# Performance work log

Measured on AMD Instinct MI355X. Metric: run time of the kernel, lower is better.

## Reference

```python
import jax, jax.numpy as jnp
import numpy as np

EPS = 1e-3  # keras LayerNormalization default epsilon


def layer_norm(x, gamma, beta):
    mu = jnp.mean(x, axis=-1, keepdims=True)
    var = jnp.mean(jnp.square(x - mu), axis=-1, keepdims=True)
    return gamma * (x - mu) * jax.lax.rsqrt(var + EPS) + beta


def setup_inputs() -> dict:
    key = jax.random.key(0)
    ks = jax.random.split(key, 5)
    B, T, E, H = 2, 2048, 64, 8
    glorot = lambda k, shape, fan_in, fan_out: jax.random.normal(k, shape, jnp.float32) * np.sqrt(2.0 / (fan_in + fan_out))
    return {
        "embedding": jax.random.normal(ks[0], (B, T, E), jnp.float32),
        "key_kernel": glorot(ks[1], (1, H, E), H, E),
        "query_kernel": glorot(ks[2], (1, H, E), H, E),
        "value_kernel": glorot(ks[3], (1, H, E, E), E, E),
        "ff_kernel": glorot(ks[4], (1, H, H, E, E), H * E, H * E),
        "ln1_gamma": jnp.ones((E,), jnp.float32),
        "ln1_beta": jnp.zeros((E,), jnp.float32),
        "ln2_gamma": jnp.ones((E,), jnp.float32),
        "ln2_beta": jnp.zeros((E,), jnp.float32),
    }


def reference(embedding, key_kernel, query_kernel, value_kernel, ff_kernel,
              ln1_gamma, ln1_beta, ln2_gamma, ln2_beta):
    # embedding: [B,T,E]; token input is expanded to [B,1,T,E] and broadcast over heads.
    kk, qk = key_kernel[0], query_kernel[0]          # [H,E]
    vk, fk = value_kernel[0], ff_kernel[0]           # [H,E,E], [H,H,E,E]
    k = jnp.einsum('bte,he->bht', embedding, kk)     # rank-1 key score per token
    q = jnp.einsum('bte,he->bht', embedding, qk)
    v = jnp.einsum('bte,hef->bhtf', embedding, vk)   # [B,H,T,E]
    scores = jnp.einsum('bhq,bhk->bhqk', q, k)       # rank-1 outer-product scores [B,H,T,T]
    attn = jax.nn.softmax(scores, axis=-1)
    z = jnp.einsum('bhqk,bhke->bhqe', attn, v)       # [B,H,T,E]
    z = embedding[:, None, :, :] + z                 # residual (broadcast over heads)
    z = layer_norm(z, ln1_gamma, ln1_beta)
    y = jnp.einsum('bhte,hgef->bgtf', z, fk)         # cross-head FFN, contracts H and E
    y = z + y
    y = jax.nn.gelu(y, approximate=True)             # tfa GELU default approximate=True
    return layer_norm(y, ln2_gamma, ln2_beta)        # [B,H,T,E]
```

## Files before the change

kernel.cpp:

```cpp
#include <hip/hip_runtime.h>
#include <math.h>

#define T 2048
#define E 64
#define H 8
#define B 2

typedef __attribute__((ext_vector_type(4))) float f32x4;
typedef __attribute__((ext_vector_type(8))) short s16x8;

static __device__ __forceinline__ unsigned short f2bf(float x) {
    union { float f; unsigned u; } v; v.f = x;
    unsigned r = v.u + 0x7FFFu + ((v.u >> 16) & 1u);
    return (unsigned short)(r >> 16);
}
static __device__ __forceinline__ float bf2f(unsigned short u) {
    union { unsigned u; float f; } v; v.u = ((unsigned)u) << 16;
    return v.f;
}
static __device__ __forceinline__ unsigned pk_bf16(float lo, float hi) {
    unsigned r;
    asm("v_cvt_pk_bf16_f32 %0, %1, %2" : "=v"(r) : "v"(lo), "v"(hi));
    return r;
}

__global__ __launch_bounds__(256) void qkvT_kernel(
    const float* __restrict__ emb,
    const float* __restrict__ qk,
    const float* __restrict__ kk,
    const float* __restrict__ vk,
    float* __restrict__ qs,
    float* __restrict__ ks,
    unsigned short* __restrict__ vT)
{
    int h  = blockIdx.x & 7;
    int tc = blockIdx.x >> 3;
    int b  = tc >> 5;
    int t0 = (tc & 31) * 64;
    int tid = threadIdx.x;

    __shared__ __align__(16) float eL[64][64];
    __shared__ __align__(16) float wkT[64*68];
    __shared__ __align__(16) unsigned short vtile[4096];

    #pragma unroll
    for (int i = 0; i < 4; ++i) {
        int s = tid + i*256;
        int t = s >> 4, e4 = s & 15;
        ((float4*)&eL[t][0])[e4] = ((const float4*)(emb + ((long)b*T + t0 + t)*E))[e4];
    }
    const float* vkh = vk + h*4096;
    #pragma unroll
    for (int i = 0; i < 16; ++i) {
        int s = tid + i*256;
        int e = s >> 6, f = s & 63;
        wkT[f*68 + e] = vkh[e*64 + f];
    }
    __syncthreads();

    if (tid < 128) {
        int t = tid & 63, sel = tid >> 6;
        const float* wp = (sel ? kk : qk) + h*64;
        float s = 0.f;
        #pragma unroll
        for (int e = 0; e < 64; ++e) {
            int ei = (e + t) & 63;
            s += eL[t][ei] * wp[ei];
        }
        float* dst = sel ? ks : qs;
        dst[((long)b*H + h)*T + t0 + t] = s;
    }

    int f  = tid & 63;
    int wv = tid >> 6;
    float acc[2][8];
    #pragma unroll
    for (int hf2 = 0; hf2 < 2; ++hf2)
        #pragma unroll
        for (int i = 0; i < 8; ++i) acc[hf2][i] = 0.f;

    #pragma unroll 4
    for (int e4 = 0; e4 < 16; ++e4) {
        float4 w4 = *(const float4*)&wkT[f*68 + e4*4];
        #pragma unroll
        for (int half = 0; half < 2; ++half) {
            int tb = half*32 + wv*8;
            #pragma unroll
            for (int i = 0; i < 8; ++i) {
                float4 ev = *(const float4*)&eL[tb + i][e4*4];
                acc[half][i] += ev.x*w4.x + ev.y*w4.y + ev.z*w4.z + ev.w*w4.w;
            }
        }
    }

    #pragma unroll
    for (int half = 0; half < 2; ++half) {
        int c = wv + half*4;
        s16x8 o;
        #pragma unroll
        for (int i = 0; i < 8; ++i) o[i] = (short)f2bf(acc[half][i]);
        *(s16x8*)&vtile[f*64 + ((c ^ (f & 7)) * 8)] = o;
    }
    __syncthreads();

    long rowbase = ((long)(b*H + h)*64) * (long)T;
    #pragma unroll
    for (int i = 0; i < 2; ++i) {
        int s = tid + i*256;
        int fo = s >> 3, c = s & 7;
        s16x8 v = *(const s16x8*)&vtile[fo*64 + ((c ^ (fo & 7)) * 8)];
        *(s16x8*)(vT + rowbase + (long)fo*T + t0 + c*8) = v;
    }
}

__global__ __launch_bounds__(256) void attn_kernel(
    const float* __restrict__ qs, const float* __restrict__ ksg,
    const unsigned short* __restrict__ vT, const float* __restrict__ emb,
    float* __restrict__ zpre)
{
    int bh = blockIdx.x >> 5;
    int q0 = (blockIdx.x & 31) * 64;
    int b  = bh >> 3;
    int tid = threadIdx.x;
    int w = tid >> 6, l = tid & 63;
    int g = l >> 4, r = l & 15;

    __shared__ __align__(16) float ksL[2048];
    __shared__ __align__(16) unsigned short VtL[2][8192];
    __shared__ float sMx[4], sMn[4];

    float4 k0 = ((const float4*)(ksg + (long)bh*T))[tid];
    float4 k1 = ((const float4*)(ksg + (long)bh*T))[tid + 256];
    ((float4*)ksL)[tid]       = k0;
    ((float4*)ksL)[tid + 256] = k1;

    float mx = fmaxf(fmaxf(fmaxf(k0.x, k0.y), fmaxf(k0.z, k0.w)),
                     fmaxf(fmaxf(k1.x, k1.y), fmaxf(k1.z, k1.w)));
    float mn = fminf(fminf(fminf(k0.x, k0.y), fminf(k0.z, k0.w)),
                     fminf(fminf(k1.x, k1.y), fminf(k1.z, k1.w)));
    #pragma unroll
    for (int o = 1; o < 64; o <<= 1) {
        mx = fmaxf(mx, __shfl_xor(mx, o, 64));
        mn = fminf(mn, __shfl_xor(mn, o, 64));
    }
    if (l == 0) { sMx[w] = mx; sMn[w] = mn; }

    float sreg = qs[(long)bh*T + q0 + w*16 + r];

    #pragma unroll
    for (int j = 0; j < 4; ++j) {
        int i = tid + j*256;
        int f = i >> 4, si = i & 15;
        s16x8 val = *(const s16x8*)(vT + ((long)(bh*64 + f))*T + si*8);
        *(s16x8*)&VtL[0][f*128 + ((si ^ (f & 15)) * 8)] = val;
    }
    __syncthreads();

    float kmx = fmaxf(fmaxf(sMx[0], sMx[1]), fmaxf(sMx[2], sMx[3]));
    float kmn = fminf(fminf(sMn[0], sMn[1]), fminf(sMn[2], sMn[3]));
    float mreg = (sreg >= 0.f) ? sreg*kmx : sreg*kmn;

    f32x4 acc[4] = {{0.f,0.f,0.f,0.f},{0.f,0.f,0.f,0.f},
                    {0.f,0.f,0.f,0.f},{0.f,0.f,0.f,0.f}};
    float dsum = 0.f;

    for (int kc = 0; kc < 16; ++kc) {
        int cur = kc & 1;
        s16x8 pf[4];
        if (kc < 15) {
            #pragma unroll
            for (int j = 0; j < 4; ++j) {
                int i = tid + j*256;
                int f = i >> 4, si = i & 15;
                pf[j] = *(const s16x8*)(vT + ((long)(bh*64 + f))*T + (kc+1)*128 + si*8);
            }
        }
        #pragma unroll
        for (int kw = 0; kw < 4; ++kw) {
            int kbase = kc*128 + kw*32 + g*8;
            float4 ka = *(const float4*)&ksL[kbase];
            float4 kb = *(const float4*)&ksL[kbase + 4];
            float p0 = __expf(fmaf(sreg, ka.x, -mreg));
            float p1 = __expf(fmaf(sreg, ka.y, -mreg));
            float p2 = __expf(fmaf(sreg, ka.z, -mreg));
            float p3 = __expf(fmaf(sreg, ka.w, -mreg));
            float p4 = __expf(fmaf(sreg, kb.x, -mreg));
            float p5 = __expf(fmaf(sreg, kb.y, -mreg));
            float p6 = __expf(fmaf(sreg, kb.z, -mreg));
            float p7 = __expf(fmaf(sreg, kb.w, -mreg));
            dsum += ((p0+p1)+(p2+p3)) + ((p4+p5)+(p6+p7));
            union { s16x8 v; unsigned u[4]; } af;
            af.u[0] = pk_bf16(p0, p1);
            af.u[1] = pk_bf16(p2, p3);
            af.u[2] = pk_bf16(p4, p5);
            af.u[3] = pk_bf16(p6, p7);
            int slot = kw*4 + g;
            #pragma unroll
            for (int ct = 0; ct < 4; ++ct) {
                s16x8 bf = *(const s16x8*)&VtL[cur][(ct*16 + r)*128 + ((slot ^ r) * 8)];
                acc[ct] = __builtin_amdgcn_mfma_f32_16x16x32_bf16(af.v, bf, acc[ct], 0, 0, 0);
            }
        }
        if (kc < 15) {
            #pragma unroll
            for (int j = 0; j < 4; ++j) {
                int i = tid + j*256;
                int f = i >> 4, si = i & 15;
                *(s16x8*)&VtL[cur ^ 1][f*128 + ((si ^ (f & 15)) * 8)] = pf[j];
            }
        }
        __syncthreads();
    }

    dsum += __shfl_xor(dsum, 16, 64);
    dsum += __shfl_xor(dsum, 32, 64);

    #pragma unroll
    for (int i = 0; i < 4; ++i) {
        int lrow = g*4 + i;
        float den = __shfl(dsum, lrow, 16);
        float inv = 1.f / den;
        long q = q0 + w*16 + lrow;
        const float* erow = emb + ((long)b*T + q)*E;
        #pragma unroll
        for (int ct = 0; ct < 4; ++ct) {
            int f = ct*16 + r;
            zpre[((long)bh*T + q)*E + f] = erow[f] + acc[ct][i] * inv;
        }
    }
}

__global__ __launch_bounds__(256) void ln1_kernel(
    const float* __restrict__ zpre,
    const float* __restrict__ g1, const float* __restrict__ b1,
    unsigned short* __restrict__ Zb)
{
    int row  = blockIdx.x*4 + (threadIdx.x >> 6);
    int lane = threadIdx.x & 63;
    float x = zpre[(long)row*64 + lane];
    float s = x, s2 = x*x;
    #pragma unroll
    for (int o = 1; o < 64; o <<= 1) {
        s  += __shfl_xor(s,  o, 64);
        s2 += __shfl_xor(s2, o, 64);
    }
    float mu  = s * (1.f/64.f);
    float var = s2 * (1.f/64.f) - mu*mu;
    float rs  = rsqrtf(var + 1e-3f);
    float zn  = g1[lane]*(x - mu)*rs + b1[lane];
    int b = row >> 14, h = (row >> 11) & 7, t = row & 2047;
    long token = (long)b*T + t;
    Zb[token*512 + h*64 + lane] = f2bf(zn);
}

__global__ __launch_bounds__(256) void wcvt_kernel(
    const float* __restrict__ fk, unsigned short* __restrict__ WbT)
{
    int hg = blockIdx.x;
    int h = hg >> 3, g = hg & 7;
    int tid = threadIdx.x;
    __shared__ float wt[64][65];
    const float* src = fk + (long)hg*4096;
    #pragma unroll
    for (int j = 0; j < 4; ++j) {
        int s = tid + j*256;
        int e = s >> 4, f4 = s & 15;
        float4 v = ((const float4*)src)[s];
        wt[e][f4*4+0] = v.x; wt[e][f4*4+1] = v.y;
        wt[e][f4*4+2] = v.z; wt[e][f4*4+3] = v.w;
    }
    __syncthreads();
    #pragma unroll
    for (int j = 0; j < 2; ++j) {
        int s = tid + j*256;
        int f = s >> 3, e8 = s & 7;
        s16x8 o;
        #pragma unroll
        for (int q = 0; q < 8; ++q) o[q] = (short)f2bf(wt[e8*8+q][f]);
        *(s16x8*)(WbT + ((long)(g*64+f))*512 + h*64 + e8*8) = o;
    }
}

__global__ __launch_bounds__(256) void ffn_gemm_kernel(
    const unsigned short* __restrict__ Zb,
    const unsigned short* __restrict__ WbT,
    const float* __restrict__ g2, const float* __restrict__ b2,
    float* __restrict__ out)
{
    int bm = blockIdx.x >> 3;
    int g  = blockIdx.x & 7;
    int m0 = bm*64;
    int tid = threadIdx.x;
    int w = tid >> 6, l = tid & 63;
    int lg = l >> 4, r = l & 15;
    int wr = w >> 1, wc = w & 1;

    __shared__ __align__(16) unsigned short As[4096];
    __shared__ __align__(16) unsigned short Bs[4096];
    __shared__ float yL[64][68];

    f32x4 acc[2][2] = {{{0.f,0.f,0.f,0.f},{0.f,0.f,0.f,0.f}},
                       {{0.f,0.f,0.f,0.f},{0.f,0.f,0.f,0.f}}};

    for (int kc = 0; kc < 8; ++kc) {
        #pragma unroll
        for (int j = 0; j < 2; ++j) {
            int s = tid + j*256;
            int row = s >> 3, c16 = s & 7;
            s16x8 va = *(const s16x8*)(Zb  + ((long)(m0 + row))*512   + kc*64 + c16*8);
            s16x8 vb = *(const s16x8*)(WbT + ((long)(g*64 + row))*512 + kc*64 + c16*8);
            *(s16x8*)&As[row*64 + ((c16 ^ (row & 7))*8)] = va;
            *(s16x8*)&Bs[row*64 + ((c16 ^ (row & 7))*8)] = vb;
        }
        __syncthreads();
        #pragma unroll
        for (int kk = 0; kk < 2; ++kk) {
            s16x8 af[2], bf[2];
            #pragma unroll
            for (int mi = 0; mi < 2; ++mi) {
                int row = wr*32 + mi*16 + r;
                af[mi] = *(const s16x8*)&As[row*64 + (((kk*4 + lg) ^ (row & 7))*8)];
            }
            #pragma unroll
            for (int ni = 0; ni < 2; ++ni) {
                int row = wc*32 + ni*16 + r;
                bf[ni] = *(const s16x8*)&Bs[row*64 + (((kk*4 + lg) ^ (row & 7))*8)];
            }
            #pragma unroll
            for (int mi = 0; mi < 2; ++mi)
                #pragma unroll
                for (int ni = 0; ni < 2; ++ni)
                    acc[mi][ni] = __builtin_amdgcn_mfma_f32_16x16x32_bf16(
                        af[mi], bf[ni], acc[mi][ni], 0, 0, 0);
        }
        __syncthreads();
    }

    #pragma unroll
    for (int mi = 0; mi < 2; ++mi)
        #pragma unroll
        for (int ni = 0; ni < 2; ++ni)
            #pragma unroll
            for (int i = 0; i < 4; ++i)
                yL[wr*32 + mi*16 + lg*4 + i][wc*32 + ni*16 + r] = acc[mi][ni][i];
    __syncthreads();

    int rowt = tid >> 2, part = tid & 3;
    const unsigned short* zrow = Zb + ((long)(m0 + rowt))*512 + g*64 + part*16;
    s16x8 z0 = *(const s16x8*)zrow;
    s16x8 z1 = *(const s16x8*)(zrow + 8);
    const float kg = 0.7978845608028654f;
    float y[16];
    float s = 0.f, s2 = 0.f;
    #pragma unroll
    for (int q = 0; q < 16; ++q) {
        float zn = bf2f((unsigned short)(q < 8 ? z0[q] : z1[q-8]));
        float x = zn + yL[rowt][part*16 + q];
        x = 0.5f*x*(1.f + tanhf(kg*(x + 0.044715f*x*x*x)));
        y[q] = x; s += x; s2 += x*x;
    }
    s  += __shfl_xor(s,  1, 64);  s  += __shfl_xor(s,  2, 64);
    s2 += __shfl_xor(s2, 1, 64);  s2 += __shfl_xor(s2, 2, 64);
    float mu  = s * (1.f/64.f);
    float var = s2 * (1.f/64.f) - mu*mu;
    float rs  = rsqrtf(var + 1e-3f);

    int token = m0 + rowt;
    int b = token >> 11, t = token & 2047;
    long ob = (((long)(b*H + g))*T + t)*64 + part*16;
    #pragma unroll
    for (int q = 0; q < 16; ++q) {
        int f = part*16 + q;
        y[q] = g2[f]*(y[q] - mu)*rs + b2[f];
    }
    #pragma unroll
    for (int q = 0; q < 4; ++q) {
        float4 o = { y[q*4], y[q*4+1], y[q*4+2], y[q*4+3] };
        *(float4*)(out + ob + q*4) = o;
    }
}

extern "C" void kernel_launch(void* const* d_in, const int* in_sizes, int n_in,
                              void* d_out, int out_size, void* d_ws, size_t ws_size,
                              hipStream_t stream) {
    const float* emb  = (const float*)d_in[0];
    const float* keyk = (const float*)d_in[1];
    const float* qryk = (const float*)d_in[2];
    const float* valk = (const float*)d_in[3];
    const float* ffk  = (const float*)d_in[4];
    const float* g1   = (const float*)d_in[5];
    const float* b1   = (const float*)d_in[6];
    const float* g2   = (const float*)d_in[7];
    const float* b2   = (const float*)d_in[8];
    float* out = (float*)d_out;

    float* ws   = (float*)d_ws;
    float* qs   = ws;
    float* ks   = ws + 32768;
    unsigned short* vT = (unsigned short*)(ws + 65568);
    float* zpre = ws + 65568 + 1048576;
    unsigned short* Zb  = vT;
    unsigned short* WbT = (unsigned short*)(ws + 65568 + 1048576 + 2097152);

    qkvT_kernel<<<(B*T/64)*H, 256, 0, stream>>>(emb, qryk, keyk, valk, qs, ks, vT);
    attn_kernel<<<B*H*(T/64), 256, 0, stream>>>(qs, ks, vT, emb, zpre);
    ln1_kernel<<<B*H*T/4, 256, 0, stream>>>(zpre, g1, b1, Zb);
    wcvt_kernel<<<H*H, 256, 0, stream>>>(ffk, WbT);
    ffn_gemm_kernel<<<(B*T/64)*H, 256, 0, stream>>>(Zb, WbT, g2, b2, out);
}
```

Measured before the change: 69.10 us.

## Split attention key dimension in two and combine partials in LN1

The attention kernel now splits the 2048 keys into two halves, launching twice as many blocks, each writing an unnormalized numerator and a denominator. The global key max/min is still computed over all keys, so both halves share the same exponent offset and can be summed directly. LN1 adds the two partials, divides, and adds the residual embedding. This doubles the grid for occupancy on a 512-block launch, at the cost of twice the intermediate numerator traffic (two fp32 partial buffers) and more workspace.

```diff
diff --git a/kernel.cpp b/kernel.cpp
--- a/kernel.cpp
+++ b/kernel.cpp
@@ -115,24 +115,25 @@
 
 __global__ __launch_bounds__(256) void attn_kernel(
     const float* __restrict__ qs, const float* __restrict__ ksg,
-    const unsigned short* __restrict__ vT, const float* __restrict__ emb,
-    float* __restrict__ zpre)
+    const unsigned short* __restrict__ vT,
+    float* __restrict__ pnum,
+    float* __restrict__ pden)
 {
-    int bh = blockIdx.x >> 5;
-    int q0 = (blockIdx.x & 31) * 64;
-    int b  = bh >> 3;
+    int bh   = blockIdx.x >> 6;
+    int rest = blockIdx.x & 63;
+    int q0   = (rest >> 1) * 64;
+    int ksp  = rest & 1;
     int tid = threadIdx.x;
     int w = tid >> 6, l = tid & 63;
     int g = l >> 4, r = l & 15;
 
-    __shared__ __align__(16) float ksL[2048];
+    __shared__ __align__(16) float ksL[1024];
     __shared__ __align__(16) unsigned short VtL[2][8192];
     __shared__ float sMx[4], sMn[4];
 
     float4 k0 = ((const float4*)(ksg + (long)bh*T))[tid];
     float4 k1 = ((const float4*)(ksg + (long)bh*T))[tid + 256];
-    ((float4*)ksL)[tid]       = k0;
-    ((float4*)ksL)[tid + 256] = k1;
+    ((float4*)ksL)[tid] = ksp ? k1 : k0;
 
     float mx = fmaxf(fmaxf(fmaxf(k0.x, k0.y), fmaxf(k0.z, k0.w)),
                      fmaxf(fmaxf(k1.x, k1.y), fmaxf(k1.z, k1.w)));
@@ -146,12 +147,13 @@
     if (l == 0) { sMx[w] = mx; sMn[w] = mn; }
 
     float sreg = qs[(long)bh*T + q0 + w*16 + r];
+    int kg0 = ksp * 8;
 
     #pragma unroll
     for (int j = 0; j < 4; ++j) {
         int i = tid + j*256;
         int f = i >> 4, si = i & 15;
-        s16x8 val = *(const s16x8*)(vT + ((long)(bh*64 + f))*T + si*8);
+        s16x8 val = *(const s16x8*)(vT + ((long)(bh*64 + f))*T + kg0*128 + si*8);
         *(s16x8*)&VtL[0][f*128 + ((si ^ (f & 15)) * 8)] = val;
     }
     __syncthreads();
@@ -164,15 +166,15 @@
                     {0.f,0.f,0.f,0.f},{0.f,0.f,0.f,0.f}};
     float dsum = 0.f;
 
-    for (int kc = 0; kc < 16; ++kc) {
+    for (int kc = 0; kc < 8; ++kc) {
         int cur = kc & 1;
         s16x8 pf[4];
-        if (kc < 15) {
+        if (kc < 7) {
             #pragma unroll
             for (int j = 0; j < 4; ++j) {
                 int i = tid + j*256;
                 int f = i >> 4, si = i & 15;
-                pf[j] = *(const s16x8*)(vT + ((long)(bh*64 + f))*T + (kc+1)*128 + si*8);
+                pf[j] = *(const s16x8*)(vT + ((long)(bh*64 + f))*T + (kg0 + kc + 1)*128 + si*8);
             }
         }
         #pragma unroll
@@ -201,7 +203,7 @@
                 acc[ct] = __builtin_amdgcn_mfma_f32_16x16x32_bf16(af.v, bf, acc[ct], 0, 0, 0);
             }
         }
-        if (kc < 15) {
+        if (kc < 7) {
             #pragma unroll
             for (int j = 0; j < 4; ++j) {
                 int i = tid + j*256;
@@ -215,29 +217,35 @@
     dsum += __shfl_xor(dsum, 16, 64);
     dsum += __shfl_xor(dsum, 32, 64);
 
+    long pbase = ((long)(ksp*16 + bh)) * T;
+    if (l < 16) pden[pbase + q0 + w*16 + l] = dsum;
+
     #pragma unroll
     for (int i = 0; i < 4; ++i) {
         int lrow = g*4 + i;
-        float den = __shfl(dsum, lrow, 16);
-        float inv = 1.f / den;
         long q = q0 + w*16 + lrow;
-        const float* erow = emb + ((long)b*T + q)*E;
-        #pragma unroll
-        for (int ct = 0; ct < 4; ++ct) {
-            int f = ct*16 + r;
-            zpre[((long)bh*T + q)*E + f] = erow[f] + acc[ct][i] * inv;
-        }
+        #pragma unroll
+        for (int ct = 0; ct < 4; ++ct)
+            pnum[(pbase + q)*64 + ct*16 + r] = acc[ct][i];
     }
 }
 
 __global__ __launch_bounds__(256) void ln1_kernel(
-    const float* __restrict__ zpre,
+    const float* __restrict__ emb,
+    const float* __restrict__ pnum, const float* __restrict__ pden,
     const float* __restrict__ g1, const float* __restrict__ b1,
     unsigned short* __restrict__ Zb)
 {
     int row  = blockIdx.x*4 + (threadIdx.x >> 6);
     int lane = threadIdx.x & 63;
-    float x = zpre[(long)row*64 + lane];
+    int bh = row >> 11, t = row & 2047;
+    int b = bh >> 3, h = bh & 7;
+    long i0 = ((long)bh)*T + t;
+    long i1 = ((long)(16 + bh))*T + t;
+    float n = pnum[i0*64 + lane] + pnum[i1*64 + lane];
+    float d = pden[i0] + pden[i1];
+    float x = emb[((long)b*T + t)*64 + lane] + n / d;
+
     float s = x, s2 = x*x;
     #pragma unroll
     for (int o = 1; o < 64; o <<= 1) {
@@ -248,9 +256,7 @@
     float var = s2 * (1.f/64.f) - mu*mu;
     float rs  = rsqrtf(var + 1e-3f);
     float zn  = g1[lane]*(x - mu)*rs + b1[lane];
-    int b = row >> 14, h = (row >> 11) & 7, t = row & 2047;
-    long token = (long)b*T + t;
-    Zb[token*512 + h*64 + lane] = f2bf(zn);
+    Zb[((long)b*T + t)*512 + h*64 + lane] = f2bf(zn);
 }
 
 __global__ __launch_bounds__(256) void wcvt_kernel(
@@ -398,13 +404,14 @@
     float* qs   = ws;
     float* ks   = ws + 32768;
     unsigned short* vT = (unsigned short*)(ws + 65568);
-    float* zpre = ws + 65568 + 1048576;
+    float* pnum = ws + 65568 + 1048576;
+    float* pden = pnum + 4194304;
     unsigned short* Zb  = vT;
-    unsigned short* WbT = (unsigned short*)(ws + 65568 + 1048576 + 2097152);
+    unsigned short* WbT = (unsigned short*)(pden + 65536);
 
     qkvT_kernel<<<(B*T/64)*H, 256, 0, stream>>>(emb, qryk, keyk, valk, qs, ks, vT);
-    attn_kernel<<<B*H*(T/64), 256, 0, stream>>>(qs, ks, vT, emb, zpre);
-    ln1_kernel<<<B*H*T/4, 256, 0, stream>>>(zpre, g1, b1, Zb);
+    attn_kernel<<<B*H*(T/64)*2, 256, 0, stream>>>(qs, ks, vT, pnum, pden);
+    ln1_kernel<<<B*H*T/4, 256, 0, stream>>>(emb, pnum, pden, g1, b1, Zb);
     wcvt_kernel<<<H*H, 256, 0, stream>>>(ffk, WbT);
     ffn_gemm_kernel<<<(B*T/64)*H, 256, 0, stream>>>(Zb, WbT, g2, b2, out);
 }
```

Result: faster. 67.64 us (-2.1%).
